# Performance work log

Measured on AMD Instinct MI355X. Metric: run time of the kernel, lower is better.

The kernel has to match this reference:

```python
import jax, jax.numpy as jnp
import numpy as np

N = 1024       # gaussians
H = 256
W = 256
C = 64         # spectral channels
K = 2          # gabor components per gaussian
RADIUS_CLIP = 1.0
CHOL_BOUND = np.array([0.5, 0.0, 0.5], dtype=np.float32)


def setup_inputs() -> dict:
    key = jax.random.key(0)
    k1, k2, k3, k4, k5 = jax.random.split(key, 5)
    # _xyz = atanh(2*(rand-0.5))
    u = jax.random.uniform(k1, (N, 2), minval=-0.999, maxval=0.999)
    xyz = jnp.arctanh(u)
    cholesky = jax.random.uniform(k2, (N, 3))
    opacity = jnp.ones((N, 1), dtype=jnp.float32)
    # features init: inverse_softplus(0.05) + 0.01*randn
    inv_sp = float(np.log(np.expm1(0.05)))
    features_dc = inv_sp + 0.01 * jax.random.normal(k3, (N, C))
    gabor_freqs = (jax.random.uniform(k4, (N * K, 2)) - 0.5) * 0.002
    gabor_weights = jax.random.uniform(k5, (N * K, 1)) * -5.0
    return {
        'xyz': xyz, 'cholesky': cholesky, 'opacity': opacity,
        'features_dc': features_dc, 'gabor_freqs': gabor_freqs,
        'gabor_weights': gabor_weights,
    }


def _render(xyz, cholesky, opacity, features_dc, gabor_freqs, gabor_weights):
    # --- project_gaussians_2d ---
    xy = jnp.tanh(xyz)                              # [N,2] in (-1,1)
    xs = 0.5 * W * (xy[:, 0] + 1.0)                 # pixel-space centers
    ys = 0.5 * H * (xy[:, 1] + 1.0)
    L = cholesky + jnp.asarray(CHOL_BOUND)[None, :]  # [N,3] -> l1,l2,l3
    l1, l2, l3 = L[:, 0], L[:, 1], L[:, 2]
    # Sigma = L L^T, L = [[l1,0],[l2,l3]]
    s11 = l1 * l1
    s12 = l1 * l2
    s22 = l2 * l2 + l3 * l3
    det = (l1 * l3) ** 2
    ca = s22 / det                                  # conic = Sigma^-1
    cb = -s12 / det
    cc = s11 / det
    # radius = ceil(3*sqrt(max eigenvalue)); prune tiny gaussians
    mid = 0.5 * (s11 + s22)
    lam_max = mid + jnp.sqrt(jnp.maximum(mid * mid - det, 1e-8))
    radius = jnp.ceil(3.0 * jnp.sqrt(lam_max))
    keep = (radius > RADIUS_CLIP).astype(xyz.dtype)  # [N]

    # --- rasterize_gabor_sum (dense reference; kernel tiles, math identical) ---
    px = jnp.arange(W, dtype=xyz.dtype) + 0.5
    py = jnp.arange(H, dtype=xyz.dtype) + 0.5
    pxf = jnp.tile(px, H)                            # [HW]
    pyf = jnp.repeat(py, W)                          # [HW]
    dx = xs[:, None] - pxf[None, :]                  # [N,HW]
    dy = ys[:, None] - pyf[None, :]
    sigma = 0.5 * (ca[:, None] * dx * dx + cc[:, None] * dy * dy) + cb[:, None] * dx * dy
    alpha = opacity * jnp.exp(-sigma) * keep[:, None]  # [N,HW]

    freqs = jnp.exp(gabor_freqs).reshape(N, K, 2)
    wts = jax.nn.sigmoid(gabor_weights).reshape(N, K)
    mod = jnp.ones_like(dx)
    for k in range(K):  # K=2, structurally small loop
        mod = mod + wts[:, k, None] * jnp.cos(freqs[:, k, 0, None] * dx + freqs[:, k, 1, None] * dy)

    wmap = alpha * mod                               # [N,HW]
    feats = jax.nn.softplus(features_dc)             # [N,C]
    out = jnp.einsum('np,nc->pc', wmap, feats)       # [HW,C], sum compositing
    out = jnp.clip(out, 0.0, 1.0)
    return out.reshape(1, H, W, C).transpose(0, 3, 1, 2)  # [1,C,H,W]


def reference(xyz, cholesky, opacity, features_dc, gabor_freqs, gabor_weights):
    return _render(xyz, cholesky, opacity, features_dc, gabor_freqs, gabor_weights)
```

## Files before the change

### kernel.cpp

```cpp
#include <hip/hip_runtime.h>
#include <hip/hip_bf16.h>

#define NG     1024
#define NC     64
#define CULL_T 15.0f
#define MAXL   256
#define APAD   258
#define L2E    1.44269504f
#define INV2PI 0.15915494f

typedef float    f32x4 __attribute__((ext_vector_type(4)));
typedef _Float16 f16x4 __attribute__((ext_vector_type(4)));
typedef _Float16 f16x2 __attribute__((ext_vector_type(2)));

__device__ __forceinline__ float wgt_f(float4 p0, float4 p1, float4 p2,
                                       float pxf, float pyf) {
    const float dx = p0.x - pxf, dy = p0.y - pyf;
    const float t  = fmaf(p0.w, dy, p0.z * dx);
    const float s2 = fmaf(p1.x * dy, dy, dx * t);
    const float e  = __builtin_amdgcn_exp2f(s2);
    const float r1 = fmaf(p2.x, dx, p2.y * dy);
    const float c1 = __builtin_amdgcn_cosf(__builtin_amdgcn_fractf(r1));
    const float r2 = fmaf(p2.z, dx, p2.w * dy);
    const float c2 = __builtin_amdgcn_cosf(__builtin_amdgcn_fractf(r2));
    const float m  = fmaf(p1.w, c2, fmaf(p1.z, c1, 1.f));
    return e * p1.y * m;
}

__global__ __launch_bounds__(1024) void fused_mfma_kernel(
    const float* __restrict__ xyz,  const float* __restrict__ chol,
    const float* __restrict__ opac, const float* __restrict__ fdc,
    const float* __restrict__ gfrq, const float* __restrict__ gwts,
    float* __restrict__ out)
{
    __shared__ float4 s_p0[MAXL], s_p1[MAXL], s_p2[MAXL];
    __shared__ unsigned short s_list[MAXL];
    __shared__ int s_scnt[16];
    __shared__ _Float16 A_lds[NC][APAD];

    const int tid  = threadIdx.x;
    const int lane = tid & 63, w = tid >> 6;

    const int x0 = (blockIdx.x & 7) << 5;
    const int y0 = (blockIdx.x >> 3) << 3;
    const float xlo = x0 + 0.5f, xhi = x0 + 31.5f;
    const float ylo = y0 + 0.5f, yhi = y0 + 7.5f;

    const int n = tid;
    const float2 xy = ((const float2*)xyz)[n];
    const float ex = __builtin_amdgcn_exp2f(2.f * L2E * xy.x);
    const float ey = __builtin_amdgcn_exp2f(2.f * L2E * xy.y);
    const float xs = 256.f - 256.f * __builtin_amdgcn_rcpf(1.f + ex);
    const float ys = 256.f - 256.f * __builtin_amdgcn_rcpf(1.f + ey);

    const float l1 = chol[3*n]     + 0.5f;
    const float l2 = chol[3*n + 1];
    const float l3 = chol[3*n + 2] + 0.5f;
    const float s11 = l1*l1, s12 = l1*l2, s22 = l2*l2 + l3*l3;
    const float dt  = (l1*l3) * (l1*l3);
    const float inv = __builtin_amdgcn_rcpf(dt);
    const float na = -0.5f * L2E * s22 * inv;
    const float nb =          L2E * s12 * inv;
    const float ncc = -0.5f * L2E * s11 * inv;
    const float mid = 0.5f * (s11 + s22);
    const float lam = mid + __builtin_amdgcn_sqrtf(fmaxf(mid*mid - dt, 1e-8f));
    const float radius = ceilf(3.f * __builtin_amdgcn_sqrtf(lam));
    const float keep = (radius > 1.0f) ? 1.f : 0.f;
    const float oK = opac[n] * keep;
    const float r2 = (oK != 0.f) ? (2.f * CULL_T * lam) : -1.f;

    const float nx = fminf(fmaxf(xs, xlo), xhi);
    const float ny = fminf(fmaxf(ys, ylo), yhi);
    const float ddx = xs - nx, ddy = ys - ny;
    const bool lv = (ddx*ddx + ddy*ddy) <= r2;

    const unsigned long long m = __ballot(lv);
    const int pos = __popcll(m & ((1ull << lane) - 1ull));
    if (lane == 0) s_scnt[w] = __popcll(m);
    __syncthreads();

    int pre[17];
    pre[0] = 0;
    #pragma unroll
    for (int s = 0; s < 16; ++s) pre[s+1] = pre[s] + s_scnt[s];
    const int total = min(pre[16], MAXL);

    if (lv) {
        const int p = pre[w] + pos;
        if (p < MAXL) {
            const float4 gf = ((const float4*)gfrq)[n];
            const float2 gw = ((const float2*)gwts)[n];
            s_list[p] = (unsigned short)n;
            s_p0[p] = make_float4(xs, ys, na, nb);
            s_p1[p] = make_float4(ncc, oK,
                __builtin_amdgcn_rcpf(1.f + __builtin_amdgcn_exp2f(-L2E*gw.x)),
                __builtin_amdgcn_rcpf(1.f + __builtin_amdgcn_exp2f(-L2E*gw.y)));
            s_p2[p] = make_float4(
                __builtin_amdgcn_exp2f(L2E*gf.x)*INV2PI,
                __builtin_amdgcn_exp2f(L2E*gf.y)*INV2PI,
                __builtin_amdgcn_exp2f(L2E*gf.z)*INV2PI,
                __builtin_amdgcn_exp2f(L2E*gf.w)*INV2PI);
        }
    }
    for (int idx = total + tid; idx < MAXL; idx += 1024) {
        s_p0[idx] = make_float4(0,0,0,0);
        s_p1[idx] = make_float4(0,0,0,0);
        s_p2[idx] = make_float4(0,0,0,0);
    }
    __syncthreads();

    const int nkc = (total + 15) >> 4;

    {
        const int c = tid & 63, kq = tid >> 6;
        for (int i = 0; i < nkc; ++i) {
            const int k0 = (i << 4) + kq;
            float v0 = 0.f;
            if (k0 < total) {
                const int nn = (int)s_list[k0];
                const float x = fdc[(nn << 6) + c];
                v0 = 0.69314718f * __builtin_amdgcn_logf(
                         1.f + __builtin_amdgcn_exp2f(L2E * x));
            }
            A_lds[c][k0] = (_Float16)v0;
        }
    }
    __syncthreads();

    const int c15 = lane & 15, g = lane >> 4;
    const float pxf = x0 + ((w & 1) << 4) + c15 + 0.5f;
    const float pyf = y0 + (w >> 1) + 0.5f;

    f32x4 acc[4];
    #pragma unroll
    for (int a = 0; a < 4; ++a) acc[a] = (f32x4){0.f,0.f,0.f,0.f};

    for (int kc = 0; kc < nkc; ++kc) {
        const int kb = (kc << 4) + (g << 2);

        const float4 q00 = s_p0[kb],   q10 = s_p1[kb],   q20 = s_p2[kb];
        const float4 q01 = s_p0[kb+1], q11 = s_p1[kb+1], q21 = s_p2[kb+1];
        const float4 q02 = s_p0[kb+2], q12 = s_p1[kb+2], q22 = s_p2[kb+2];
        const float4 q03 = s_p0[kb+3], q13 = s_p1[kb+3], q23 = s_p2[kb+3];

        const f16x4 bf = {
            (_Float16)wgt_f(q00, q10, q20, pxf, pyf),
            (_Float16)wgt_f(q01, q11, q21, pxf, pyf),
            (_Float16)wgt_f(q02, q12, q22, pxf, pyf),
            (_Float16)wgt_f(q03, q13, q23, pxf, pyf) };

        const f16x4 af0 = *(const f16x4*)&A_lds[ 0 + c15][kb];
        const f16x4 af1 = *(const f16x4*)&A_lds[16 + c15][kb];
        const f16x4 af2 = *(const f16x4*)&A_lds[32 + c15][kb];
        const f16x4 af3 = *(const f16x4*)&A_lds[48 + c15][kb];

        acc[0] = __builtin_amdgcn_mfma_f32_16x16x16f16(af0, bf, acc[0], 0,0,0);
        acc[1] = __builtin_amdgcn_mfma_f32_16x16x16f16(af1, bf, acc[1], 0,0,0);
        acc[2] = __builtin_amdgcn_mfma_f32_16x16x16f16(af2, bf, acc[2], 0,0,0);
        acc[3] = __builtin_amdgcn_mfma_f32_16x16x16f16(af3, bf, acc[3], 0,0,0);
    }

    const int pg = ((y0 + (w >> 1)) << 8) + x0 + ((w & 1) << 4) + c15;
    #pragma unroll
    for (int mt = 0; mt < 4; ++mt) {
        #pragma unroll
        for (int q = 0; q < 4; ++q) {
            const int ch = mt*16 + g*4 + q;
            __builtin_nontemporal_store(
                fminf(fmaxf(acc[mt][q], 0.f), 1.f), &out[(ch << 16) + pg]);
        }
    }
}

extern "C" void kernel_launch(void* const* d_in, const int* in_sizes, int n_in,
                              void* d_out, int out_size, void* d_ws, size_t ws_size,
                              hipStream_t stream) {
    const float* xyz  = (const float*)d_in[0];
    const float* chol = (const float*)d_in[1];
    const float* opac = (const float*)d_in[2];
    const float* fdc  = (const float*)d_in[3];
    const float* gfrq = (const float*)d_in[4];
    const float* gwts = (const float*)d_in[5];

    fused_mfma_kernel<<<256, 1024, 0, stream>>>(xyz, chol, opac, fdc,
                                                gfrq, gwts, (float*)d_out);
}
```

Measured before the change: 11.30 us.

## Halve pixel tile to 16x8 with 512-thread blocks, two gaussians per thread

Shrinks each block's tile from 32x8 to 16x8 pixels and launches 512 blocks of 512 threads. Each thread now projects and culls two gaussians, keeping the same compaction order. Feature softplus staging writes two halves per thread. This raises block count and shrinks per-tile gaussian lists for better CU balance, at the cost of duplicating the projection work across twice as many blocks.

```diff
diff --git a/kernel.cpp b/kernel.cpp
--- a/kernel.cpp
+++ b/kernel.cpp
@@ -27,7 +27,7 @@
     return e * p1.y * m;
 }
 
-__global__ __launch_bounds__(1024) void fused_mfma_kernel(
+__global__ __launch_bounds__(512, 4) void fused_mfma_kernel(
     const float* __restrict__ xyz,  const float* __restrict__ chol,
     const float* __restrict__ opac, const float* __restrict__ fdc,
     const float* __restrict__ gfrq, const float* __restrict__ gwts,
@@ -41,42 +41,52 @@
     const int tid  = threadIdx.x;
     const int lane = tid & 63, w = tid >> 6;
 
-    const int x0 = (blockIdx.x & 7) << 5;
-    const int y0 = (blockIdx.x >> 3) << 3;
-    const float xlo = x0 + 0.5f, xhi = x0 + 31.5f;
+    const int x0 = (blockIdx.x & 15) << 4;
+    const int y0 = (blockIdx.x >> 4) << 3;
+    const float xlo = x0 + 0.5f, xhi = x0 + 15.5f;
     const float ylo = y0 + 0.5f, yhi = y0 + 7.5f;
 
-    const int n = tid;
-    const float2 xy = ((const float2*)xyz)[n];
-    const float ex = __builtin_amdgcn_exp2f(2.f * L2E * xy.x);
-    const float ey = __builtin_amdgcn_exp2f(2.f * L2E * xy.y);
-    const float xs = 256.f - 256.f * __builtin_amdgcn_rcpf(1.f + ex);
-    const float ys = 256.f - 256.f * __builtin_amdgcn_rcpf(1.f + ey);
-
-    const float l1 = chol[3*n]     + 0.5f;
-    const float l2 = chol[3*n + 1];
-    const float l3 = chol[3*n + 2] + 0.5f;
-    const float s11 = l1*l1, s12 = l1*l2, s22 = l2*l2 + l3*l3;
-    const float dt  = (l1*l3) * (l1*l3);
-    const float inv = __builtin_amdgcn_rcpf(dt);
-    const float na = -0.5f * L2E * s22 * inv;
-    const float nb =          L2E * s12 * inv;
-    const float ncc = -0.5f * L2E * s11 * inv;
-    const float mid = 0.5f * (s11 + s22);
-    const float lam = mid + __builtin_amdgcn_sqrtf(fmaxf(mid*mid - dt, 1e-8f));
-    const float radius = ceilf(3.f * __builtin_amdgcn_sqrtf(lam));
-    const float keep = (radius > 1.0f) ? 1.f : 0.f;
-    const float oK = opac[n] * keep;
-    const float r2 = (oK != 0.f) ? (2.f * CULL_T * lam) : -1.f;
-
-    const float nx = fminf(fmaxf(xs, xlo), xhi);
-    const float ny = fminf(fmaxf(ys, ylo), yhi);
-    const float ddx = xs - nx, ddy = ys - ny;
-    const bool lv = (ddx*ddx + ddy*ddy) <= r2;
-
-    const unsigned long long m = __ballot(lv);
-    const int pos = __popcll(m & ((1ull << lane) - 1ull));
-    if (lane == 0) s_scnt[w] = __popcll(m);
+    float4 P0[2];
+    float  NCC[2], OK[2];
+    bool   lv[2];
+    int    pos[2];
+    #pragma unroll
+    for (int r = 0; r < 2; ++r) {
+        const int n = (r << 9) + tid;
+        const float2 xy = ((const float2*)xyz)[n];
+        const float ex = __builtin_amdgcn_exp2f(2.f * L2E * xy.x);
+        const float ey = __builtin_amdgcn_exp2f(2.f * L2E * xy.y);
+        const float xs = 256.f - 256.f * __builtin_amdgcn_rcpf(1.f + ex);
+        const float ys = 256.f - 256.f * __builtin_amdgcn_rcpf(1.f + ey);
+
+        const float l1 = chol[3*n]     + 0.5f;
+        const float l2 = chol[3*n + 1];
+        const float l3 = chol[3*n + 2] + 0.5f;
+        const float s11 = l1*l1, s12 = l1*l2, s22 = l2*l2 + l3*l3;
+        const float dt  = (l1*l3) * (l1*l3);
+        const float inv = __builtin_amdgcn_rcpf(dt);
+        const float na = -0.5f * L2E * s22 * inv;
+        const float nb =          L2E * s12 * inv;
+        const float nc = -0.5f * L2E * s11 * inv;
+        const float mid = 0.5f * (s11 + s22);
+        const float lam = mid + __builtin_amdgcn_sqrtf(fmaxf(mid*mid - dt, 1e-8f));
+        const float radius = ceilf(3.f * __builtin_amdgcn_sqrtf(lam));
+        const float keep = (radius > 1.0f) ? 1.f : 0.f;
+        const float oK = opac[n] * keep;
+        const float r2 = (oK != 0.f) ? (2.f * CULL_T * lam) : -1.f;
+
+        const float nx = fminf(fmaxf(xs, xlo), xhi);
+        const float ny = fminf(fmaxf(ys, ylo), yhi);
+        const float ddx = xs - nx, ddy = ys - ny;
+        lv[r] = (ddx*ddx + ddy*ddy) <= r2;
+
+        const unsigned long long m = __ballot(lv[r]);
+        pos[r] = __popcll(m & ((1ull << lane) - 1ull));
+        if (lane == 0) s_scnt[(r << 3) + w] = __popcll(m);
+
+        P0[r] = make_float4(xs, ys, na, nb);
+        NCC[r] = nc; OK[r] = oK;
+    }
     __syncthreads();
 
     int pre[17];
@@ -85,24 +95,28 @@
     for (int s = 0; s < 16; ++s) pre[s+1] = pre[s] + s_scnt[s];
     const int total = min(pre[16], MAXL);
 
-    if (lv) {
-        const int p = pre[w] + pos;
-        if (p < MAXL) {
-            const float4 gf = ((const float4*)gfrq)[n];
-            const float2 gw = ((const float2*)gwts)[n];
-            s_list[p] = (unsigned short)n;
-            s_p0[p] = make_float4(xs, ys, na, nb);
-            s_p1[p] = make_float4(ncc, oK,
-                __builtin_amdgcn_rcpf(1.f + __builtin_amdgcn_exp2f(-L2E*gw.x)),
-                __builtin_amdgcn_rcpf(1.f + __builtin_amdgcn_exp2f(-L2E*gw.y)));
-            s_p2[p] = make_float4(
-                __builtin_amdgcn_exp2f(L2E*gf.x)*INV2PI,
-                __builtin_amdgcn_exp2f(L2E*gf.y)*INV2PI,
-                __builtin_amdgcn_exp2f(L2E*gf.z)*INV2PI,
-                __builtin_amdgcn_exp2f(L2E*gf.w)*INV2PI);
+    #pragma unroll
+    for (int r = 0; r < 2; ++r) {
+        if (lv[r]) {
+            const int p = pre[(r << 3) + w] + pos[r];
+            if (p < MAXL) {
+                const int n = (r << 9) + tid;
+                const float4 gf = ((const float4*)gfrq)[n];
+                const float2 gw = ((const float2*)gwts)[n];
+                s_list[p] = (unsigned short)n;
+                s_p0[p] = P0[r];
+                s_p1[p] = make_float4(NCC[r], OK[r],
+                    __builtin_amdgcn_rcpf(1.f + __builtin_amdgcn_exp2f(-L2E*gw.x)),
+                    __builtin_amdgcn_rcpf(1.f + __builtin_amdgcn_exp2f(-L2E*gw.y)));
+                s_p2[p] = make_float4(
+                    __builtin_amdgcn_exp2f(L2E*gf.x)*INV2PI,
+                    __builtin_amdgcn_exp2f(L2E*gf.y)*INV2PI,
+                    __builtin_amdgcn_exp2f(L2E*gf.z)*INV2PI,
+                    __builtin_amdgcn_exp2f(L2E*gf.w)*INV2PI);
+            }
         }
     }
-    for (int idx = total + tid; idx < MAXL; idx += 1024) {
+    for (int idx = total + tid; idx < MAXL; idx += 512) {
         s_p0[idx] = make_float4(0,0,0,0);
         s_p1[idx] = make_float4(0,0,0,0);
         s_p2[idx] = make_float4(0,0,0,0);
@@ -114,22 +128,28 @@
     {
         const int c = tid & 63, kq = tid >> 6;
         for (int i = 0; i < nkc; ++i) {
-            const int k0 = (i << 4) + kq;
-            float v0 = 0.f;
+            const int k0 = (i << 4) + (kq << 1);
+            float v0 = 0.f, v1 = 0.f;
             if (k0 < total) {
                 const int nn = (int)s_list[k0];
                 const float x = fdc[(nn << 6) + c];
                 v0 = 0.69314718f * __builtin_amdgcn_logf(
                          1.f + __builtin_amdgcn_exp2f(L2E * x));
             }
-            A_lds[c][k0] = (_Float16)v0;
+            if (k0 + 1 < total) {
+                const int nn = (int)s_list[k0 + 1];
+                const float x = fdc[(nn << 6) + c];
+                v1 = 0.69314718f * __builtin_amdgcn_logf(
+                         1.f + __builtin_amdgcn_exp2f(L2E * x));
+            }
+            *(f16x2*)&A_lds[c][k0] = (f16x2){(_Float16)v0, (_Float16)v1};
         }
     }
     __syncthreads();
 
     const int c15 = lane & 15, g = lane >> 4;
-    const float pxf = x0 + ((w & 1) << 4) + c15 + 0.5f;
-    const float pyf = y0 + (w >> 1) + 0.5f;
+    const float pxf = x0 + c15 + 0.5f;
+    const float pyf = y0 + w + 0.5f;
 
     f32x4 acc[4];
     #pragma unroll
@@ -160,7 +180,7 @@
         acc[3] = __builtin_amdgcn_mfma_f32_16x16x16f16(af3, bf, acc[3], 0,0,0);
     }
 
-    const int pg = ((y0 + (w >> 1)) << 8) + x0 + ((w & 1) << 4) + c15;
+    const int pg = ((y0 + w) << 8) + x0 + c15;
     #pragma unroll
     for (int mt = 0; mt < 4; ++mt) {
         #pragma unroll
@@ -182,6 +202,6 @@
     const float* gfrq = (const float*)d_in[4];
     const float* gwts = (const float*)d_in[5];
 
-    fused_mfma_kernel<<<256, 1024, 0, stream>>>(xyz, chol, opac, fdc,
-                                                gfrq, gwts, (float*)d_out);
+    fused_mfma_kernel<<<512, 512, 0, stream>>>(xyz, chol, opac, fdc,
+                                               gfrq, gwts, (float*)d_out);
 }
```

Result: slower. 12.26 us (+8.5%).
